# Optimization experiments

Hardware: AMD Instinct MI355X
Metric: run time of the kernel (lower is better)

Reference implementation:

```python
import jax, jax.numpy as jnp
import numpy as np

NUM_USERS = 100000
NUM_ITEMS = 100000
D = 64
C = 9          # cat_num (9 attention layers)
B = 2048       # batch of users
L = 200        # max history length (padded with -1)
H = 16         # attention MLP hidden size


def setup_inputs() -> dict:
    key = jax.random.key(0)
    ks = jax.random.split(key, 12)
    w_range = np.sqrt(3.0 / D).astype(np.float32)

    user_inputs = jax.random.randint(ks[0], (B,), 0, NUM_USERS)
    record = jax.random.randint(ks[1], (B, L), 0, NUM_ITEMS)
    # ragged lengths: pad tail with -1 (original code breaks at -1)
    lengths = jax.random.randint(ks[2], (B, 1), L // 4, L + 1)
    record_inputs = jnp.where(jnp.arange(L)[None, :] < lengths, record, -1)
    item_inputs = jax.random.randint(ks[3], (B,), 0, NUM_ITEMS)
    item_cat = jax.random.randint(ks[4], (NUM_ITEMS,), 0, C)

    user_emb = 0.01 * jax.random.normal(ks[5], (NUM_USERS, D), jnp.float32)
    item_emb = 0.01 * jax.random.normal(ks[6], (NUM_ITEMS, D), jnp.float32)
    W1 = jax.random.uniform(ks[7], (C, H, 2 * D), jnp.float32, -w_range, w_range)
    b1 = jnp.zeros((C, H), jnp.float32)
    W2 = jax.random.uniform(ks[8], (C, 1, H), jnp.float32, -w_range, w_range)
    b2 = jnp.zeros((C, 1), jnp.float32)
    Wt1 = jax.random.uniform(ks[9], (H, 2 * D), jnp.float32, -w_range, w_range)
    bt1 = jnp.zeros((H,), jnp.float32)
    Wt2 = jax.random.uniform(ks[10], (1, H), jnp.float32, -w_range, w_range)
    bt2 = jnp.zeros((1,), jnp.float32)

    return {"user_inputs": user_inputs, "record_inputs": record_inputs,
            "item_inputs": item_inputs, "item_cat": item_cat,
            "user_emb": user_emb, "item_emb": item_emb,
            "W1": W1, "b1": b1, "W2": W2, "b2": b2,
            "Wt1": Wt1, "bt1": bt1, "Wt2": Wt2, "bt2": bt2}


def _forward(user_inputs, record_inputs, item_inputs, item_cat,
             user_emb, item_emb, W1, b1, W2, b2, Wt1, bt1, Wt2, bt2):
    tiny = jnp.asarray(1e-30, jnp.float32)
    valid = record_inputs >= 0                     # [B,L]
    rec = jnp.where(valid, record_inputs, 0)
    e = item_emb[rec]                              # [B,L,D]
    u = user_emb[user_inputs]                      # [B,D]
    x = jnp.concatenate([jnp.broadcast_to(u[:, None, :], e.shape), e], -1)  # [B,L,2D]

    # per-category attention MLP scores (C small -> compute all, gather by cat)
    h = jax.nn.relu(jnp.einsum('chi,bli->bclh', W1, x) + b1[None, :, None, :])  # [B,C,L,H]
    s = jnp.einsum('ch,bclh->bcl', W2[:, 0, :], h) + b2[:, 0][None, :, None]    # [B,C,L]

    cat = item_cat[rec]                                            # [B,L]
    member = (cat[:, None, :] == jnp.arange(C)[None, :, None]) & valid[:, None, :]  # [B,C,L]

    # masked softmax within each (user, category) group
    smax = jnp.max(jnp.where(member, s, -jnp.inf), axis=-1, keepdims=True)
    smax = jnp.where(jnp.isfinite(smax), smax, 0.0)
    z = jnp.where(member, jnp.exp(s - smax), 0.0)
    w = z / jnp.maximum(jnp.sum(z, -1, keepdims=True), tiny)       # [B,C,L]
    gvec = jnp.einsum('bcl,bld->bcd', w, e)                        # [B,C,D]
    group_has = jnp.any(member, axis=-1)                           # [B,C]

    # top-level attention over non-empty groups
    x2 = jnp.concatenate([jnp.broadcast_to(u[:, None, :], gvec.shape), gvec], -1)  # [B,C,2D]
    h2 = jax.nn.relu(jnp.einsum('hi,bci->bch', Wt1, x2) + bt1)      # [B,C,H]
    s2 = jnp.einsum('h,bch->bc', Wt2[0], h2) + bt2[0]               # [B,C]
    s2max = jnp.max(jnp.where(group_has, s2, -jnp.inf), -1, keepdims=True)
    s2max = jnp.where(jnp.isfinite(s2max), s2max, 0.0)
    z2 = jnp.where(group_has, jnp.exp(s2 - s2max), 0.0)
    w2 = z2 / jnp.maximum(jnp.sum(z2, -1, keepdims=True), tiny)
    hybrid = jnp.einsum('bc,bcd->bd', w2, gvec)                     # [B,D]

    ti = item_emb[item_inputs]                                      # [B,D]
    return jnp.sum(hybrid * ti, -1).reshape(-1, 1, 1)               # [B,1,1]


def reference(user_inputs, record_inputs, item_inputs, item_cat,
              user_emb, item_emb, W1, b1, W2, b2, Wt1, bt1, Wt2, bt2):
    return _forward(user_inputs, record_inputs, item_inputs, item_cat,
                    user_emb, item_emb, W1, b1, W2, b2, Wt1, bt1, Wt2, bt2)
```

## Files before the change

### kernel.cpp

```cpp
#include <hip/hip_runtime.h>
#include <math.h>

#define NB 2048
#define LL 200
#define PADL 256
#define DD 64
#define CC 9
#define HH 16
#define NW 4


__global__ __launch_bounds__(256) void din_k1(
    const int* __restrict__ user_inputs,
    const int* __restrict__ record_inputs,
    const int* __restrict__ item_cat,
    const float* __restrict__ user_emb,
    const float* __restrict__ item_emb,
    const float* __restrict__ W1,
    const float* __restrict__ b1,
    const float* __restrict__ W2,
    const float* __restrict__ b2,
    int* __restrict__ srow_g,
    float* __restrict__ z_g,
    int* __restrict__ cstart_g)
{
  const int b = blockIdx.x;
  const int t = threadIdx.x;
  const int wave = t >> 6, lane = t & 63;

  __shared__ float4 w_lds[HH * 16 * CC];
  __shared__ float  w2_s[CC * HH];
  __shared__ float  b2_s[CC];
  __shared__ float  u_s[DD];
  __shared__ float  pre_s[CC][HH];
  __shared__ int    wcnt[NW][CC];
  __shared__ int    cstart[CC + 1];
  __shared__ int    ccnt[CC];
  __shared__ int    srow_sh[PADL];

  #pragma unroll
  for (int k = t; k < HH * 16 * CC; k += 256) {
    int c = k >> 8;
    int ji = k & 255;
    int j = ji >> 4, i = ji & 15;
    w_lds[ji * CC + c] = ((const float4*)W1)[(size_t)(c * HH + j) * 32 + 16 + i];
  }
  if (t < CC * HH) w2_s[t] = W2[t];
  if (t < CC) b2_s[t] = b2[t];

  int r = -1, c0 = -1;
  if (t < LL) {
    r = record_inputs[b * LL + t];
    if (r >= 0) c0 = item_cat[r];
  }
  if (t < DD) u_s[t] = user_emb[(size_t)user_inputs[b] * DD + t];
  srow_sh[t] = 0;
  srow_g[b * PADL + t] = 0;

  int myrank = 0;
  #pragma unroll
  for (int c = 0; c < CC; ++c) {
    unsigned long long m = __ballot(c0 == c);
    if (lane == 0) wcnt[wave][c] = __popcll(m);
    if (c0 == c) myrank = __popcll(m & ((1ULL << lane) - 1ULL));
  }
  __syncthreads();

  if (t == 0) {
    int acc = 0;
    #pragma unroll
    for (int c = 0; c < CC; ++c) {
      cstart[c] = acc;
      int cn = wcnt[0][c] + wcnt[1][c] + wcnt[2][c] + wcnt[3][c];
      ccnt[c] = cn;
      acc = (acc + cn + 3) & ~3;
    }
    cstart[CC] = acc;
  }
  if (t < CC * HH) {
    int c = t / HH, j = t % HH;
    const float* wp = &W1[(size_t)(c * HH + j) * (2 * DD)];
    float acc = b1[c * HH + j];
    #pragma unroll 8
    for (int d = 0; d < DD; ++d) acc += wp[d] * u_s[d];
    pre_s[c][j] = acc;
  }
  __syncthreads();

  if (c0 >= 0) {
    int off = cstart[c0];
    for (int w = 0; w < wave; ++w) off += wcnt[w][c0];
    int pos = off + myrank;
    srow_sh[pos] = r;
    srow_g[b * PADL + pos] = r;
  }
  if (t < CC + 1) cstart_g[b * 20 + t] = cstart[t];
  else if (t < 2 * CC + 1) cstart_g[b * 20 + 10 + (t - CC - 1)] = ccnt[t - CC - 1];
  __syncthreads();

  const int ntot = cstart[CC];
  const int grp  = t >> 2;
  const int jq   = t & 3;
  const int q4   = grp * 4;
  if (q4 < ntot) {
    int c = 0;
    #pragma unroll
    for (int q = 0; q < CC - 1; ++q) c += (q4 >= cstart[q + 1]) ? 1 : 0;

    const int r0 = srow_sh[q4 + 0], r1 = srow_sh[q4 + 1];
    const int r2 = srow_sh[q4 + 2], r3 = srow_sh[q4 + 3];
    const float4* e0 = (const float4*)&item_emb[(size_t)r0 * DD];
    const float4* e1 = (const float4*)&item_emb[(size_t)r1 * DD];
    const float4* e2 = (const float4*)&item_emb[(size_t)r2 * DD];
    const float4* e3 = (const float4*)&item_emb[(size_t)r3 * DD];

    float acc0[4], acc1[4], acc2[4], acc3[4];
    #pragma unroll
    for (int jj = 0; jj < 4; ++jj) {
      float pv = pre_s[c][jq * 4 + jj];
      acc0[jj] = pv; acc1[jj] = pv; acc2[jj] = pv; acc3[jj] = pv;
    }

    #pragma unroll
    for (int i = 0; i < 16; ++i) {
      float4 a0 = e0[i], a1 = e1[i], a2 = e2[i], a3 = e3[i];
      #pragma unroll
      for (int jj = 0; jj < 4; ++jj) {
        float4 wv = w_lds[((jq * 4 + jj) * 16 + i) * CC + c];
        acc0[jj] += wv.x * a0.x + wv.y * a0.y + wv.z * a0.z + wv.w * a0.w;
        acc1[jj] += wv.x * a1.x + wv.y * a1.y + wv.z * a1.z + wv.w * a1.w;
        acc2[jj] += wv.x * a2.x + wv.y * a2.y + wv.z * a2.z + wv.w * a2.w;
        acc3[jj] += wv.x * a3.x + wv.y * a3.y + wv.z * a3.z + wv.w * a3.w;
      }
    }

    float s0 = 0.f, s1 = 0.f, s2 = 0.f, s3 = 0.f;
    #pragma unroll
    for (int jj = 0; jj < 4; ++jj) {
      float w2v = w2_s[c * HH + jq * 4 + jj];
      s0 += w2v * fmaxf(acc0[jj], 0.f);
      s1 += w2v * fmaxf(acc1[jj], 0.f);
      s2 += w2v * fmaxf(acc2[jj], 0.f);
      s3 += w2v * fmaxf(acc3[jj], 0.f);
    }
    s0 += __shfl_xor(s0, 1, 64); s0 += __shfl_xor(s0, 2, 64);
    s1 += __shfl_xor(s1, 1, 64); s1 += __shfl_xor(s1, 2, 64);
    s2 += __shfl_xor(s2, 1, 64); s2 += __shfl_xor(s2, 2, 64);
    s3 += __shfl_xor(s3, 1, 64); s3 += __shfl_xor(s3, 2, 64);

    if (jq == 0) {
      const float b2c = b2_s[c];
      *(float4*)&z_g[b * PADL + q4] = make_float4(expf(s0 + b2c), expf(s1 + b2c),
                                                  expf(s2 + b2c), expf(s3 + b2c));
    }
  }
}

__global__ __launch_bounds__(256) void din_kcd(
    const int* __restrict__ user_inputs,
    const int* __restrict__ item_inputs,
    const float* __restrict__ user_emb,
    const float* __restrict__ item_emb,
    const float* __restrict__ Wt1,
    const float* __restrict__ bt1,
    const float* __restrict__ Wt2,
    const float* __restrict__ bt2,
    const int* __restrict__ srow_g,
    const float* __restrict__ z_g,
    const int* __restrict__ cstart_g,
    float* __restrict__ out)
{
  const int b = blockIdx.x;
  const int t = threadIdx.x;
  const int wave = t >> 6, lane = t & 63;
  const int g = lane >> 4;
  const int h = lane & 15;

  __shared__ float u_s[DD];
  __shared__ float gvec_s[CC][DD];
  __shared__ float h2_s[CC][HH];
  __shared__ float w2t_s[CC];
  __shared__ int   cnt_s[CC];

  if (t < DD) u_s[t] = user_emb[(size_t)user_inputs[b] * DD + t];

  for (int c = wave; c < CC; c += NW) {
    const int i0 = cstart_g[b * 20 + c];
    const int n  = cstart_g[b * 20 + 10 + c];
    if (lane == 0) cnt_s[c] = n;
    const int sb = b * PADL + i0;

    float4 acc = make_float4(0.f, 0.f, 0.f, 0.f);
    float  zs  = 0.f;

    for (int cb = 0; cb < n; cb += 64) {
      const int nn = min(64, n - cb);
      const bool ok = (cb + lane) < n;
      int   rv = ok ? srow_g[sb + cb + lane] : 0;
      float zv = ok ? z_g[sb + cb + lane]    : 0.f;
      zs += zv;

      const int kmax = (nn + 3) >> 2;
      #pragma unroll 4
      for (int k = 0; k < kmax; ++k) {
        const int j = 4 * k + g;
        const int   rr = __shfl(rv, j, 64);
        const float zz = __shfl(zv, j, 64);
        const float4 ev = *(const float4*)&item_emb[(size_t)rr * DD + 4 * h];
        acc.x += zz * ev.x; acc.y += zz * ev.y;
        acc.z += zz * ev.z; acc.w += zz * ev.w;
      }
    }

    acc.x += __shfl_xor(acc.x, 16, 64); acc.y += __shfl_xor(acc.y, 16, 64);
    acc.z += __shfl_xor(acc.z, 16, 64); acc.w += __shfl_xor(acc.w, 16, 64);
    acc.x += __shfl_xor(acc.x, 32, 64); acc.y += __shfl_xor(acc.y, 32, 64);
    acc.z += __shfl_xor(acc.z, 32, 64); acc.w += __shfl_xor(acc.w, 32, 64);
    #pragma unroll
    for (int off = 32; off > 0; off >>= 1) zs += __shfl_xor(zs, off, 64);

    if (g == 0) {
      const float inv = 1.f / fmaxf(zs, 1e-30f);
      gvec_s[c][4 * h + 0] = acc.x * inv;
      gvec_s[c][4 * h + 1] = acc.y * inv;
      gvec_s[c][4 * h + 2] = acc.z * inv;
      gvec_s[c][4 * h + 3] = acc.w * inv;
    }
  }
  __syncthreads();

  if (t < CC * HH) {
    int cc = t / HH, j = t % HH;
    const float* wp = &Wt1[(size_t)j * (2 * DD)];
    float a = bt1[j];
    #pragma unroll 8
    for (int d = 0; d < DD; ++d) a += wp[d] * u_s[d];
    #pragma unroll 8
    for (int d = 0; d < DD; ++d) a += wp[DD + d] * gvec_s[cc][d];
    h2_s[cc][j] = fmaxf(a, 0.f);
  }
  __syncthreads();

  if (t == 0) {
    float s2[CC];
    float m = -INFINITY;
    #pragma unroll
    for (int cc = 0; cc < CC; ++cc) {
      float a = bt2[0];
      #pragma unroll
      for (int j = 0; j < HH; ++j) a += Wt2[j] * h2_s[cc][j];
      s2[cc] = a;
      if (cnt_s[cc] > 0) m = fmaxf(m, a);
    }
    if (m == -INFINITY) m = 0.f;
    float sum = 0.f;
    float z2[CC];
    #pragma unroll
    for (int cc = 0; cc < CC; ++cc) {
      z2[cc] = (cnt_s[cc] > 0) ? expf(s2[cc] - m) : 0.f;
      sum += z2[cc];
    }
    float inv = 1.f / fmaxf(sum, 1e-30f);
    #pragma unroll
    for (int cc = 0; cc < CC; ++cc) w2t_s[cc] = z2[cc] * inv;
  }
  __syncthreads();

  if (t < DD) {
    float hy = 0.f;
    #pragma unroll
    for (int cc = 0; cc < CC; ++cc) hy += w2t_s[cc] * gvec_s[cc][t];
    float ti = item_emb[(size_t)item_inputs[b] * DD + t];
    float prod = hy * ti;
    #pragma unroll
    for (int off = 32; off > 0; off >>= 1)
      prod += __shfl_down(prod, off, 64);
    if (t == 0) out[b] = prod;
  }
}

extern "C" void kernel_launch(void* const* d_in, const int* in_sizes, int n_in,
                              void* d_out, int out_size, void* d_ws, size_t ws_size,
                              hipStream_t stream) {
  const int*   user_inputs   = (const int*)d_in[0];
  const int*   record_inputs = (const int*)d_in[1];
  const int*   item_inputs   = (const int*)d_in[2];
  const int*   item_cat      = (const int*)d_in[3];
  const float* user_emb      = (const float*)d_in[4];
  const float* item_emb      = (const float*)d_in[5];
  const float* W1            = (const float*)d_in[6];
  const float* b1            = (const float*)d_in[7];
  const float* W2            = (const float*)d_in[8];
  const float* b2            = (const float*)d_in[9];
  const float* Wt1           = (const float*)d_in[10];
  const float* bt1           = (const float*)d_in[11];
  const float* Wt2           = (const float*)d_in[12];
  const float* bt2           = (const float*)d_in[13];
  float* out = (float*)d_out;

  char* ws = (char*)d_ws;
  int*   srow_g   = (int*)(ws);
  float* z_g      = (float*)(ws + 2097152);
  int*   cstart_g = (int*)(ws + 4194304);

  din_k1<<<NB, 256, 0, stream>>>(user_inputs, record_inputs, item_cat,
                                 user_emb, item_emb, W1, b1, W2, b2,
                                 srow_g, z_g, cstart_g);
  din_kcd<<<NB, 256, 0, stream>>>(user_inputs, item_inputs, user_emb, item_emb,
                                  Wt1, bt1, Wt2, bt2,
                                  srow_g, z_g, cstart_g, out);
}
```

Measured before the change: 70.38 us.

## Fuse scoring and pooling kernels into one block-per-user kernel

Merges the two kernels into a single kernel that keeps the sorted record rows, per-item attention weights and category offsets in shared memory instead of writing them to a global workspace and reading them back. This removes one launch, the global round-trip of srow/z/cstart, and the cross-lane shuffles used to broadcast rows. It also XOR-swizzles the W1 float4 layout in LDS to reduce bank conflicts. In exchange the fused kernel uses more shared memory per block, which may lower occupancy.

```diff
diff --git a/kernel.cpp b/kernel.cpp
--- a/kernel.cpp
+++ b/kernel.cpp
@@ -9,10 +9,10 @@
 #define HH 16
 #define NW 4
 
-
-__global__ __launch_bounds__(256) void din_k1(
+__global__ __launch_bounds__(256) void din_fused(
     const int* __restrict__ user_inputs,
     const int* __restrict__ record_inputs,
+    const int* __restrict__ item_inputs,
     const int* __restrict__ item_cat,
     const float* __restrict__ user_emb,
     const float* __restrict__ item_emb,
@@ -20,9 +20,11 @@
     const float* __restrict__ b1,
     const float* __restrict__ W2,
     const float* __restrict__ b2,
-    int* __restrict__ srow_g,
-    float* __restrict__ z_g,
-    int* __restrict__ cstart_g)
+    const float* __restrict__ Wt1,
+    const float* __restrict__ bt1,
+    const float* __restrict__ Wt2,
+    const float* __restrict__ bt2,
+    float* __restrict__ out)
 {
   const int b = blockIdx.x;
   const int t = threadIdx.x;
@@ -37,13 +39,18 @@
   __shared__ int    cstart[CC + 1];
   __shared__ int    ccnt[CC];
   __shared__ int    srow_sh[PADL];
+  __shared__ float  z_s[PADL];
+  __shared__ float  gvec_s[CC][DD];
+  __shared__ float  h2_s[CC][HH];
+  __shared__ float  w2t_s[CC];
 
   #pragma unroll
   for (int k = t; k < HH * 16 * CC; k += 256) {
     int c = k >> 8;
     int ji = k & 255;
     int j = ji >> 4, i = ji & 15;
-    w_lds[ji * CC + c] = ((const float4*)W1)[(size_t)(c * HH + j) * 32 + 16 + i];
+    int phys = (ji * CC + c) ^ ((ji >> 6) << 1);
+    w_lds[phys] = ((const float4*)W1)[(size_t)(c * HH + j) * 32 + 16 + i];
   }
   if (t < CC * HH) w2_s[t] = W2[t];
   if (t < CC) b2_s[t] = b2[t];
@@ -55,7 +62,6 @@
   }
   if (t < DD) u_s[t] = user_emb[(size_t)user_inputs[b] * DD + t];
   srow_sh[t] = 0;
-  srow_g[b * PADL + t] = 0;
 
   int myrank = 0;
   #pragma unroll
@@ -90,141 +96,101 @@
   if (c0 >= 0) {
     int off = cstart[c0];
     for (int w = 0; w < wave; ++w) off += wcnt[w][c0];
-    int pos = off + myrank;
-    srow_sh[pos] = r;
-    srow_g[b * PADL + pos] = r;
-  }
-  if (t < CC + 1) cstart_g[b * 20 + t] = cstart[t];
-  else if (t < 2 * CC + 1) cstart_g[b * 20 + 10 + (t - CC - 1)] = ccnt[t - CC - 1];
+    srow_sh[off + myrank] = r;
+  }
   __syncthreads();
 
   const int ntot = cstart[CC];
-  const int grp  = t >> 2;
-  const int jq   = t & 3;
-  const int q4   = grp * 4;
-  if (q4 < ntot) {
-    int c = 0;
-    #pragma unroll
-    for (int q = 0; q < CC - 1; ++q) c += (q4 >= cstart[q + 1]) ? 1 : 0;
-
-    const int r0 = srow_sh[q4 + 0], r1 = srow_sh[q4 + 1];
-    const int r2 = srow_sh[q4 + 2], r3 = srow_sh[q4 + 3];
-    const float4* e0 = (const float4*)&item_emb[(size_t)r0 * DD];
-    const float4* e1 = (const float4*)&item_emb[(size_t)r1 * DD];
-    const float4* e2 = (const float4*)&item_emb[(size_t)r2 * DD];
-    const float4* e3 = (const float4*)&item_emb[(size_t)r3 * DD];
-
-    float acc0[4], acc1[4], acc2[4], acc3[4];
-    #pragma unroll
-    for (int jj = 0; jj < 4; ++jj) {
-      float pv = pre_s[c][jq * 4 + jj];
-      acc0[jj] = pv; acc1[jj] = pv; acc2[jj] = pv; acc3[jj] = pv;
-    }
-
-    #pragma unroll
-    for (int i = 0; i < 16; ++i) {
-      float4 a0 = e0[i], a1 = e1[i], a2 = e2[i], a3 = e3[i];
+  {
+    const int grp = t >> 2, jq = t & 3;
+    const int q4 = grp * 4;
+    if (q4 < ntot) {
+      int c = 0;
+      #pragma unroll
+      for (int q = 0; q < CC - 1; ++q) c += (q4 >= cstart[q + 1]) ? 1 : 0;
+
+      const int r0 = srow_sh[q4 + 0], r1 = srow_sh[q4 + 1];
+      const int r2 = srow_sh[q4 + 2], r3 = srow_sh[q4 + 3];
+      const float4* e0 = (const float4*)&item_emb[(size_t)r0 * DD];
+      const float4* e1 = (const float4*)&item_emb[(size_t)r1 * DD];
+      const float4* e2 = (const float4*)&item_emb[(size_t)r2 * DD];
+      const float4* e3 = (const float4*)&item_emb[(size_t)r3 * DD];
+
+      float acc0[4], acc1[4], acc2[4], acc3[4];
       #pragma unroll
       for (int jj = 0; jj < 4; ++jj) {
-        float4 wv = w_lds[((jq * 4 + jj) * 16 + i) * CC + c];
-        acc0[jj] += wv.x * a0.x + wv.y * a0.y + wv.z * a0.z + wv.w * a0.w;
-        acc1[jj] += wv.x * a1.x + wv.y * a1.y + wv.z * a1.z + wv.w * a1.w;
-        acc2[jj] += wv.x * a2.x + wv.y * a2.y + wv.z * a2.z + wv.w * a2.w;
-        acc3[jj] += wv.x * a3.x + wv.y * a3.y + wv.z * a3.z + wv.w * a3.w;
-      }
-    }
-
-    float s0 = 0.f, s1 = 0.f, s2 = 0.f, s3 = 0.f;
-    #pragma unroll
-    for (int jj = 0; jj < 4; ++jj) {
-      float w2v = w2_s[c * HH + jq * 4 + jj];
-      s0 += w2v * fmaxf(acc0[jj], 0.f);
-      s1 += w2v * fmaxf(acc1[jj], 0.f);
-      s2 += w2v * fmaxf(acc2[jj], 0.f);
-      s3 += w2v * fmaxf(acc3[jj], 0.f);
-    }
-    s0 += __shfl_xor(s0, 1, 64); s0 += __shfl_xor(s0, 2, 64);
-    s1 += __shfl_xor(s1, 1, 64); s1 += __shfl_xor(s1, 2, 64);
-    s2 += __shfl_xor(s2, 1, 64); s2 += __shfl_xor(s2, 2, 64);
-    s3 += __shfl_xor(s3, 1, 64); s3 += __shfl_xor(s3, 2, 64);
-
-    if (jq == 0) {
-      const float b2c = b2_s[c];
-      *(float4*)&z_g[b * PADL + q4] = make_float4(expf(s0 + b2c), expf(s1 + b2c),
-                                                  expf(s2 + b2c), expf(s3 + b2c));
-    }
-  }
-}
-
-__global__ __launch_bounds__(256) void din_kcd(
-    const int* __restrict__ user_inputs,
-    const int* __restrict__ item_inputs,
-    const float* __restrict__ user_emb,
-    const float* __restrict__ item_emb,
-    const float* __restrict__ Wt1,
-    const float* __restrict__ bt1,
-    const float* __restrict__ Wt2,
-    const float* __restrict__ bt2,
-    const int* __restrict__ srow_g,
-    const float* __restrict__ z_g,
-    const int* __restrict__ cstart_g,
-    float* __restrict__ out)
-{
-  const int b = blockIdx.x;
-  const int t = threadIdx.x;
-  const int wave = t >> 6, lane = t & 63;
-  const int g = lane >> 4;
-  const int h = lane & 15;
-
-  __shared__ float u_s[DD];
-  __shared__ float gvec_s[CC][DD];
-  __shared__ float h2_s[CC][HH];
-  __shared__ float w2t_s[CC];
-  __shared__ int   cnt_s[CC];
-
-  if (t < DD) u_s[t] = user_emb[(size_t)user_inputs[b] * DD + t];
-
-  for (int c = wave; c < CC; c += NW) {
-    const int i0 = cstart_g[b * 20 + c];
-    const int n  = cstart_g[b * 20 + 10 + c];
-    if (lane == 0) cnt_s[c] = n;
-    const int sb = b * PADL + i0;
-
-    float4 acc = make_float4(0.f, 0.f, 0.f, 0.f);
-    float  zs  = 0.f;
-
-    for (int cb = 0; cb < n; cb += 64) {
-      const int nn = min(64, n - cb);
-      const bool ok = (cb + lane) < n;
-      int   rv = ok ? srow_g[sb + cb + lane] : 0;
-      float zv = ok ? z_g[sb + cb + lane]    : 0.f;
-      zs += zv;
-
-      const int kmax = (nn + 3) >> 2;
+        float pv = pre_s[c][jq * 4 + jj];
+        acc0[jj] = pv; acc1[jj] = pv; acc2[jj] = pv; acc3[jj] = pv;
+      }
+
+      #pragma unroll
+      for (int i = 0; i < 16; ++i) {
+        float4 a0 = e0[i], a1 = e1[i], a2 = e2[i], a3 = e3[i];
+        #pragma unroll
+        for (int jj = 0; jj < 4; ++jj) {
+          int ji = (jq * 4 + jj) * 16 + i;
+          float4 wv = w_lds[(ji * CC + c) ^ (jq << 1)];
+          acc0[jj] += wv.x * a0.x + wv.y * a0.y + wv.z * a0.z + wv.w * a0.w;
+          acc1[jj] += wv.x * a1.x + wv.y * a1.y + wv.z * a1.z + wv.w * a1.w;
+          acc2[jj] += wv.x * a2.x + wv.y * a2.y + wv.z * a2.z + wv.w * a2.w;
+          acc3[jj] += wv.x * a3.x + wv.y * a3.y + wv.z * a3.z + wv.w * a3.w;
+        }
+      }
+
+      float s0 = 0.f, s1 = 0.f, s2 = 0.f, s3 = 0.f;
+      #pragma unroll
+      for (int jj = 0; jj < 4; ++jj) {
+        float w2v = w2_s[c * HH + jq * 4 + jj];
+        s0 += w2v * fmaxf(acc0[jj], 0.f);
+        s1 += w2v * fmaxf(acc1[jj], 0.f);
+        s2 += w2v * fmaxf(acc2[jj], 0.f);
+        s3 += w2v * fmaxf(acc3[jj], 0.f);
+      }
+      s0 += __shfl_xor(s0, 1, 64); s0 += __shfl_xor(s0, 2, 64);
+      s1 += __shfl_xor(s1, 1, 64); s1 += __shfl_xor(s1, 2, 64);
+      s2 += __shfl_xor(s2, 1, 64); s2 += __shfl_xor(s2, 2, 64);
+      s3 += __shfl_xor(s3, 1, 64); s3 += __shfl_xor(s3, 2, 64);
+
+      if (jq == 0) {
+        const float b2c = b2_s[c];
+        *(float4*)&z_s[q4] = make_float4(expf(s0 + b2c), expf(s1 + b2c),
+                                         expf(s2 + b2c), expf(s3 + b2c));
+      }
+    }
+  }
+  __syncthreads();
+
+  {
+    const int g = lane >> 4, h = lane & 15;
+    for (int c = wave; c < CC; c += NW) {
+      const int i0 = cstart[c], n = ccnt[c];
+      float4 acc = make_float4(0.f, 0.f, 0.f, 0.f);
+      float  zs  = 0.f;
+      const int kmax = (n + 3) >> 2;
       #pragma unroll 4
       for (int k = 0; k < kmax; ++k) {
-        const int j = 4 * k + g;
-        const int   rr = __shfl(rv, j, 64);
-        const float zz = __shfl(zv, j, 64);
+        const int io = 4 * k + g;
+        const int rr = srow_sh[i0 + io];
+        const float zz = (io < n) ? z_s[i0 + io] : 0.f;
         const float4 ev = *(const float4*)&item_emb[(size_t)rr * DD + 4 * h];
         acc.x += zz * ev.x; acc.y += zz * ev.y;
         acc.z += zz * ev.z; acc.w += zz * ev.w;
-      }
-    }
-
-    acc.x += __shfl_xor(acc.x, 16, 64); acc.y += __shfl_xor(acc.y, 16, 64);
-    acc.z += __shfl_xor(acc.z, 16, 64); acc.w += __shfl_xor(acc.w, 16, 64);
-    acc.x += __shfl_xor(acc.x, 32, 64); acc.y += __shfl_xor(acc.y, 32, 64);
-    acc.z += __shfl_xor(acc.z, 32, 64); acc.w += __shfl_xor(acc.w, 32, 64);
-    #pragma unroll
-    for (int off = 32; off > 0; off >>= 1) zs += __shfl_xor(zs, off, 64);
-
-    if (g == 0) {
-      const float inv = 1.f / fmaxf(zs, 1e-30f);
-      gvec_s[c][4 * h + 0] = acc.x * inv;
-      gvec_s[c][4 * h + 1] = acc.y * inv;
-      gvec_s[c][4 * h + 2] = acc.z * inv;
-      gvec_s[c][4 * h + 3] = acc.w * inv;
+        zs += zz;
+      }
+      acc.x += __shfl_xor(acc.x, 16, 64); acc.y += __shfl_xor(acc.y, 16, 64);
+      acc.z += __shfl_xor(acc.z, 16, 64); acc.w += __shfl_xor(acc.w, 16, 64);
+      acc.x += __shfl_xor(acc.x, 32, 64); acc.y += __shfl_xor(acc.y, 32, 64);
+      acc.z += __shfl_xor(acc.z, 32, 64); acc.w += __shfl_xor(acc.w, 32, 64);
+      zs += __shfl_xor(zs, 16, 64);
+      zs += __shfl_xor(zs, 32, 64);
+
+      if (g == 0) {
+        const float inv = 1.f / fmaxf(zs, 1e-30f);
+        gvec_s[c][4 * h + 0] = acc.x * inv;
+        gvec_s[c][4 * h + 1] = acc.y * inv;
+        gvec_s[c][4 * h + 2] = acc.z * inv;
+        gvec_s[c][4 * h + 3] = acc.w * inv;
+      }
     }
   }
   __syncthreads();
@@ -250,14 +216,14 @@
       #pragma unroll
       for (int j = 0; j < HH; ++j) a += Wt2[j] * h2_s[cc][j];
       s2[cc] = a;
-      if (cnt_s[cc] > 0) m = fmaxf(m, a);
+      if (ccnt[cc] > 0) m = fmaxf(m, a);
     }
     if (m == -INFINITY) m = 0.f;
     float sum = 0.f;
     float z2[CC];
     #pragma unroll
     for (int cc = 0; cc < CC; ++cc) {
-      z2[cc] = (cnt_s[cc] > 0) ? expf(s2[cc] - m) : 0.f;
+      z2[cc] = (ccnt[cc] > 0) ? expf(s2[cc] - m) : 0.f;
       sum += z2[cc];
     }
     float inv = 1.f / fmaxf(sum, 1e-30f);
@@ -298,15 +264,7 @@
   const float* bt2           = (const float*)d_in[13];
   float* out = (float*)d_out;
 
-  char* ws = (char*)d_ws;
-  int*   srow_g   = (int*)(ws);
-  float* z_g      = (float*)(ws + 2097152);
-  int*   cstart_g = (int*)(ws + 4194304);
-
-  din_k1<<<NB, 256, 0, stream>>>(user_inputs, record_inputs, item_cat,
-                                 user_emb, item_emb, W1, b1, W2, b2,
-                                 srow_g, z_g, cstart_g);
-  din_kcd<<<NB, 256, 0, stream>>>(user_inputs, item_inputs, user_emb, item_emb,
-                                  Wt1, bt1, Wt2, bt2,
-                                  srow_g, z_g, cstart_g, out);
+  din_fused<<<NB, 256, 0, stream>>>(user_inputs, record_inputs, item_inputs,
+                                    item_cat, user_emb, item_emb,
+                                    W1, b1, W2, b2, Wt1, bt1, Wt2, bt2, out);
 }
```

New measurement: 70.19 us. Within noise of the previous version (-0.3%).
